# Kernel tuning notes

Measured on AMD Instinct MI355X. Metric: run time of the kernel, lower is better.

## Reference

```python
import jax, jax.numpy as jnp
import numpy as np

EPS = 1e-12

def _sn(w, u):
    # spectral norm, num_svs=1, num_itrs=1, eval mode (power iteration is
    # under no_grad in the original, so sv is a constant w.r.t. autodiff)
    Wm = w.reshape(w.shape[0], -1)          # [out, in*kh*kw]
    v = u @ Wm                               # [1, in*kh*kw]
    v = v / jnp.maximum(jnp.linalg.norm(v), EPS)
    u2 = v @ Wm.T                            # [1, out]
    u2 = u2 / jnp.maximum(jnp.linalg.norm(u2), EPS)
    sv = jnp.squeeze(v @ Wm.T @ u2.T)        # top singular value estimate
    return w / jax.lax.stop_gradient(sv)


def setup_inputs() -> dict:
    key = jax.random.key(0)
    ks = jax.random.split(key, 10)
    B, C, H, W = 32, 512, 64, 64
    Cr = C // 8
    return {
        'x':  jax.random.normal(ks[0], (B, C, H, W), jnp.float32),
        'w1': jax.random.normal(ks[1], (Cr, C, 1, 1), jnp.float32) * 0.05,
        'b1': jax.random.normal(ks[2], (Cr,), jnp.float32) * 0.02,
        'u1': jax.random.normal(ks[3], (1, Cr), jnp.float32),
        'w2': jax.random.normal(ks[4], (C, Cr, 1, 1), jnp.float32) * 0.05,
        'b2': jax.random.normal(ks[5], (C,), jnp.float32) * 0.02,
        'u2': jax.random.normal(ks[6], (1, C), jnp.float32),
        'w3': jax.random.normal(ks[7], (1, 2, 3, 3), jnp.float32) * 0.1,
        'b3': jax.random.normal(ks[8], (1,), jnp.float32) * 0.02,
        'u3': jax.random.normal(ks[9], (1, 1), jnp.float32),
    }


def reference(x, w1, b1, u1, w2, b2, u2, w3, b3, u3):
    # --- channel attention ---
    W1 = _sn(w1, u1).reshape(w1.shape[0], w1.shape[1])   # [Cr, C]
    W2 = _sn(w2, u2).reshape(w2.shape[0], w2.shape[1])   # [C, Cr]
    avg = jnp.mean(x, axis=(2, 3))                        # [B, C]
    mx  = jnp.max(x, axis=(2, 3))                         # [B, C]
    a = jax.nn.relu(avg @ W1.T + b1) @ W2.T + b2          # [B, C]
    m = jax.nn.relu(mx  @ W1.T + b1) @ W2.T + b2          # [B, C]
    s = jax.nn.sigmoid(a + m)
    x = x * s[:, :, None, None]
    # --- spatial attention ---
    ca = jnp.mean(x, axis=1, keepdims=True)               # [B,1,H,W]
    cm = jnp.max(x, axis=1, keepdims=True)                # [B,1,H,W]
    cat = jnp.concatenate([ca, cm], axis=1)               # [B,2,H,W]
    W3 = _sn(w3, u3)
    y = jax.lax.conv_general_dilated(
        cat, W3, window_strides=(1, 1), padding=((1, 1), (1, 1)),
        dimension_numbers=('NCHW', 'OIHW', 'NCHW'))
    y = y + b3.reshape(1, -1, 1, 1)
    return x * jax.nn.sigmoid(y)
```

## Files before the change

### kernel.cpp

```cpp
#include <hip/hip_runtime.h>


#define B_   32
#define C_   512
#define CR_  64
#define HW_  4096
#define WID_ 64
#define EPSF 1e-12f

__device__ __forceinline__ float sigmoidf(float x) {
  return 1.0f / (1.0f + __expf(-x));
}

__global__ __launch_bounds__(256) void pool_kernel(const float* __restrict__ x,
                                                   float* __restrict__ avg,
                                                   float* __restrict__ mx) {
  const int plane = blockIdx.x * 4 + (threadIdx.x >> 6);
  const int lane = threadIdx.x & 63;
  const float4* xp = (const float4*)(x + (size_t)plane * HW_);
  float s = 0.0f, m = -INFINITY;
  #pragma unroll
  for (int q = 0; q < 16; q++) {
    float4 a = xp[q * 64 + lane];
    s += (a.x + a.y) + (a.z + a.w);
    m = fmaxf(m, fmaxf(fmaxf(a.x, a.y), fmaxf(a.z, a.w)));
  }
  #pragma unroll
  for (int o = 32; o > 0; o >>= 1) {
    s += __shfl_down(s, o);
    m = fmaxf(m, __shfl_down(m, o));
  }
  if (lane == 0) {
    avg[plane] = s * (1.0f / HW_);
    mx[plane] = m;
  }
}

__device__ __forceinline__ float block_reduce_sum(float v, float* red) {
  int t = threadIdx.x;
  red[t] = v;
  __syncthreads();
  for (int o = 128; o > 0; o >>= 1) {
    if (t < o) red[t] += red[t + o];
    __syncthreads();
  }
  float r = red[0];
  __syncthreads();
  return r;
}

__global__ __launch_bounds__(256) void mlp_kernel(const float* __restrict__ avg, const float* __restrict__ mx,
                                                  const float* __restrict__ w1, const float* __restrict__ b1,
                                                  const float* __restrict__ u1,
                                                  const float* __restrict__ w2, const float* __restrict__ b2,
                                                  const float* __restrict__ u2,
                                                  float* __restrict__ s) {
  const int b = blockIdx.y;
  const int qtr = blockIdx.x;
  const int t = threadIdx.x;
  __shared__ float v[C_];
  __shared__ float red[256];
  __shared__ float pool2[2][C_];
  __shared__ float hid[2][CR_];

  if (t < CR_) hid[0][t] = u1[t];
  __syncthreads();
  float ax = 0.0f, ay = 0.0f;
  #pragma unroll 8
  for (int i = 0; i < CR_; i++) {
    float ui = hid[0][i];
    float2 wv = *(const float2*)(w1 + (size_t)i * C_ + 2 * t);
    ax += ui * wv.x; ay += ui * wv.y;
  }
  v[2 * t] = ax; v[2 * t + 1] = ay;
  float nv = block_reduce_sum(ax * ax + ay * ay, red);
  float dv = fmaxf(sqrtf(nv), EPSF);
  {
    int i = t >> 2, part = t & 3;
    const float4* wr = (const float4*)(w1 + (size_t)i * C_ + part * 128);
    float acc = 0.0f;
    #pragma unroll 8
    for (int q = 0; q < 32; q++) {
      float4 wv = wr[q];
      int j = part * 128 + 4 * q;
      acc += v[j] * wv.x + v[j + 1] * wv.y + v[j + 2] * wv.z + v[j + 3] * wv.w;
    }
    acc += __shfl_down(acc, 2);
    acc += __shfl_down(acc, 1);
    float q2 = 0.0f;
    if (part == 0) { float a2 = acc / dv; q2 = a2 * a2; }
    nv = block_reduce_sum(q2, red);
  }
  const float inv1 = fmaxf(sqrtf(nv), EPSF) / nv;

  for (int i = t; i < C_; i += 256) pool2[0][i] = u2[i];
  __syncthreads();
  {
    int j = t & 63, ig = t >> 6;
    const float* wp = w2 + (size_t)ig * 128 * CR_ + j;
    float a = 0.0f;
    #pragma unroll 8
    for (int i = 0; i < 128; i++) a += pool2[0][ig * 128 + i] * wp[(size_t)i * CR_];
    red[t] = a;
  }
  __syncthreads();
  if (t < CR_) v[t] = red[t] + red[t + 64] + red[t + 128] + red[t + 192];
  __syncthreads();
  float p = (t < CR_) ? v[t] * v[t] : 0.0f;
  nv = block_reduce_sum(p, red);
  dv = fmaxf(sqrtf(nv), EPSF);
  {
    float q = 0.0f;
    #pragma unroll
    for (int rep = 0; rep < 2; rep++) {
      int i = t + rep * 256;
      const float4* wr = (const float4*)(w2 + (size_t)i * CR_);
      float acc = 0.0f;
      #pragma unroll
      for (int qq = 0; qq < 16; qq++) {
        float4 wv = wr[qq];
        acc += v[4 * qq] * wv.x + v[4 * qq + 1] * wv.y +
               v[4 * qq + 2] * wv.z + v[4 * qq + 3] * wv.w;
      }
      acc /= dv;
      q += acc * acc;
    }
    nv = block_reduce_sum(q, red);
  }
  const float inv2 = fmaxf(sqrtf(nv), EPSF) / nv;

  for (int i = t; i < C_; i += 256) {
    pool2[0][i] = avg[b * C_ + i];
    pool2[1][i] = mx[b * C_ + i];
  }
  __syncthreads();
  if (t < 2 * CR_) {
    int kind = t >> 6;
    int i = t & 63;
    const float4* wr = (const float4*)(w1 + (size_t)i * C_);
    float acc = 0.0f;
    #pragma unroll 8
    for (int qq = 0; qq < C_ / 4; qq++) {
      float4 u = wr[qq];
      acc += pool2[kind][qq * 4 + 0] * u.x + pool2[kind][qq * 4 + 1] * u.y +
             pool2[kind][qq * 4 + 2] * u.z + pool2[kind][qq * 4 + 3] * u.w;
    }
    hid[kind][i] = fmaxf(acc * inv1 + b1[i], 0.0f);
  }
  __syncthreads();
  if (t < 128) {
    int c = qtr * 128 + t;
    const float4* wr = (const float4*)(w2 + (size_t)c * CR_);
    float aa = 0.0f, mm = 0.0f;
    #pragma unroll
    for (int k = 0; k < 16; k++) {
      float4 wv = wr[k];
      aa += hid[0][4 * k] * wv.x + hid[0][4 * k + 1] * wv.y +
            hid[0][4 * k + 2] * wv.z + hid[0][4 * k + 3] * wv.w;
      mm += hid[1][4 * k] * wv.x + hid[1][4 * k + 1] * wv.y +
            hid[1][4 * k + 2] * wv.z + hid[1][4 * k + 3] * wv.w;
    }
    float val = (aa + mm) * inv2 + 2.0f * b2[c];
    s[b * C_ + c] = sigmoidf(val);
  }
}

__global__ __launch_bounds__(256) void scale_pool_kernel(const float* __restrict__ x,
                                                         const float* __restrict__ s,
                                                         float* __restrict__ ca,
                                                         float* __restrict__ cm) {
  const int b = blockIdx.y;
  const int hw0 = blockIdx.x * 128;
  const int t = threadIdx.x;
  const int pxs = t & 31;
  const int cg = t >> 5;
  __shared__ float srow[C_];
  for (int i = t; i < C_; i += 256) srow[i] = s[b * C_ + i];
  __syncthreads();
  const int px = hw0 + pxs * 4;
  const float* xb = x + (size_t)b * C_ * HW_ + px;
  float4 sm = make_float4(0.f, 0.f, 0.f, 0.f);
  float4 mxv = make_float4(-INFINITY, -INFINITY, -INFINITY, -INFINITY);
  const int c0 = cg * 64;
  #pragma unroll 8
  for (int c = c0; c < c0 + 64; c++) {
    float4 u = *(const float4*)(xb + (size_t)c * HW_);
    float sc = srow[c];
    float v0 = u.x * sc, v1 = u.y * sc, v2 = u.z * sc, v3 = u.w * sc;
    sm.x += v0; sm.y += v1; sm.z += v2; sm.w += v3;
    mxv.x = fmaxf(mxv.x, v0); mxv.y = fmaxf(mxv.y, v1);
    mxv.z = fmaxf(mxv.z, v2); mxv.w = fmaxf(mxv.w, v3);
  }
  __shared__ float4 rs[8][32], rm[8][32];
  rs[cg][pxs] = sm; rm[cg][pxs] = mxv;
  __syncthreads();
  if (t < 32) {
    float4 S = rs[0][t], M = rm[0][t];
    #pragma unroll
    for (int g = 1; g < 8; g++) {
      float4 a = rs[g][t], m2 = rm[g][t];
      S.x += a.x; S.y += a.y; S.z += a.z; S.w += a.w;
      M.x = fmaxf(M.x, m2.x); M.y = fmaxf(M.y, m2.y);
      M.z = fmaxf(M.z, m2.z); M.w = fmaxf(M.w, m2.w);
    }
    S.x *= (1.0f / C_); S.y *= (1.0f / C_); S.z *= (1.0f / C_); S.w *= (1.0f / C_);
    *(float4*)(ca + (size_t)b * HW_ + hw0 + t * 4) = S;
    *(float4*)(cm + (size_t)b * HW_ + hw0 + t * 4) = M;
  }
}

__global__ __launch_bounds__(256) void conv_sy_kernel(const float* __restrict__ ca,
                                                      const float* __restrict__ cm,
                                                      const float* __restrict__ w3,
                                                      const float* __restrict__ b3,
                                                      const float* __restrict__ u3,
                                                      float* __restrict__ sy) {
  const int b = blockIdx.y;
  const int hw0 = blockIdx.x * 512;
  const int t = threadIdx.x;
  __shared__ float ssv3;
  if (t == 0) {
    float u3v = u3[0];
    float nvs = 0.0f;
    for (int k = 0; k < 18; k++) { float vv = u3v * w3[k]; nvs += vv * vv; }
    float d = fmaxf(sqrtf(nvs), EPSF);
    float tt = 0.0f;
    for (int k = 0; k < 18; k++) tt += (u3v * w3[k] / d) * w3[k];
    float u2n = tt / fmaxf(fabsf(tt), EPSF);
    ssv3 = tt * u2n;
  }
  __syncthreads();
  const float inv3 = 1.0f / ssv3;
  float wn[18];
  #pragma unroll
  for (int k = 0; k < 18; k++) wn[k] = w3[k] * inv3;
  const float b3f = b3[0];

  #pragma unroll
  for (int e = 0; e < 2; e++) {
    int px = hw0 + t * 2 + e;
    int h = px >> 6, w = px & 63;
    float acc = b3f;
    #pragma unroll
    for (int dh = -1; dh <= 1; dh++) {
      int hh = h + dh;
      if (hh < 0 || hh >= 64) continue;
      #pragma unroll
      for (int dw = -1; dw <= 1; dw++) {
        int ww = w + dw;
        if (ww < 0 || ww >= WID_) continue;
        int n = b * HW_ + hh * WID_ + ww;
        int k = (dh + 1) * 3 + (dw + 1);
        acc += ca[n] * wn[k] + cm[n] * wn[9 + k];
      }
    }
    sy[b * HW_ + px] = sigmoidf(acc);
  }
}

__global__ __launch_bounds__(256) void out_kernel(const float* __restrict__ x,
                                                  const float* __restrict__ s,
                                                  const float* __restrict__ sy,
                                                  float* __restrict__ out) {
  const size_t N4 = (size_t)B_ * C_ * HW_ / 4;
  const size_t stride = (size_t)gridDim.x * blockDim.x;
  for (size_t i = (size_t)blockIdx.x * blockDim.x + threadIdx.x; i < N4; i += stride) {
    size_t base = i * 4;
    int hw = (int)(base & (HW_ - 1));
    int bc = (int)(base >> 12);
    int b  = bc >> 9;
    float sc = s[bc];
    float4 u = ((const float4*)x)[i];
    float4 g = *(const float4*)(sy + (size_t)b * HW_ + hw);
    float4 r;
    r.x = u.x * sc * g.x;
    r.y = u.y * sc * g.y;
    r.z = u.z * sc * g.z;
    r.w = u.w * sc * g.w;
    ((float4*)out)[i] = r;
  }
}

extern "C" void kernel_launch(void* const* d_in, const int* in_sizes, int n_in,
                              void* d_out, int out_size, void* d_ws, size_t ws_size,
                              hipStream_t stream) {
  const float* x  = (const float*)d_in[0];
  const float* w1 = (const float*)d_in[1];
  const float* b1 = (const float*)d_in[2];
  const float* u1 = (const float*)d_in[3];
  const float* w2 = (const float*)d_in[4];
  const float* b2 = (const float*)d_in[5];
  const float* u2 = (const float*)d_in[6];
  const float* w3 = (const float*)d_in[7];
  const float* b3 = (const float*)d_in[8];
  const float* u3 = (const float*)d_in[9];

  float* ws = (float*)d_ws;
  float* avg = ws;
  float* mx  = ws + 16384;
  float* s   = ws + 32768;
  float* ca  = ws + 49152;
  float* cm  = ws + 180224;
  float* sy  = ws + 311296;

  pool_kernel<<<B_ * C_ / 4, 256, 0, stream>>>(x, avg, mx);
  mlp_kernel<<<dim3(4, B_), 256, 0, stream>>>(avg, mx, w1, b1, u1, w2, b2, u2, s);
  scale_pool_kernel<<<dim3(32, B_), 256, 0, stream>>>(x, s, ca, cm);
  conv_sy_kernel<<<dim3(8, B_), 256, 0, stream>>>(ca, cm, w3, b3, u3, sy);
  out_kernel<<<2048, 256, 0, stream>>>(x, s, sy, (float*)d_out);
}
```

Before: 583.7 us.

## Fuse spatial conv with output scaling and parallelize spectral-norm power iterations

Merges the 3x3 spatial conv/sigmoid kernel into the final output kernel, so each block computes its 128-pixel tile of sy in shared memory and then streams x to out with nontemporal vector loads and stores. This removes one launch and the sy round trip through global memory. The MLP kernel also runs the two spectral-norm power iterations concurrently on the two halves of the block, with split reductions that need fewer barriers. The conv work now uses only half the threads per block and repeats the spectral-norm setup in every block.

```diff
diff --git a/kernel.cpp b/kernel.cpp
--- a/kernel.cpp
+++ b/kernel.cpp
@@ -7,6 +7,8 @@
 #define HW_  4096
 #define WID_ 64
 #define EPSF 1e-12f
+
+typedef float f32x4 __attribute__((ext_vector_type(4)));
 
 __device__ __forceinline__ float sigmoidf(float x) {
   return 1.0f / (1.0f + __expf(-x));
@@ -36,19 +38,6 @@
   }
 }
 
-__device__ __forceinline__ float block_reduce_sum(float v, float* red) {
-  int t = threadIdx.x;
-  red[t] = v;
-  __syncthreads();
-  for (int o = 128; o > 0; o >>= 1) {
-    if (t < o) red[t] += red[t + o];
-    __syncthreads();
-  }
-  float r = red[0];
-  __syncthreads();
-  return r;
-}
-
 __global__ __launch_bounds__(256) void mlp_kernel(const float* __restrict__ avg, const float* __restrict__ mx,
                                                   const float* __restrict__ w1, const float* __restrict__ b1,
                                                   const float* __restrict__ u1,
@@ -58,85 +47,104 @@
   const int b = blockIdx.y;
   const int qtr = blockIdx.x;
   const int t = threadIdx.x;
-  __shared__ float v[C_];
+  __shared__ float v1[C_];
+  __shared__ float v2[CR_];
   __shared__ float red[256];
+  __shared__ float part2[128];
+  __shared__ float u1s[CR_];
+  __shared__ float u2s[C_];
   __shared__ float pool2[2][C_];
   __shared__ float hid[2][CR_];
 
-  if (t < CR_) hid[0][t] = u1[t];
-  __syncthreads();
-  float ax = 0.0f, ay = 0.0f;
-  #pragma unroll 8
-  for (int i = 0; i < CR_; i++) {
-    float ui = hid[0][i];
-    float2 wv = *(const float2*)(w1 + (size_t)i * C_ + 2 * t);
-    ax += ui * wv.x; ay += ui * wv.y;
-  }
-  v[2 * t] = ax; v[2 * t + 1] = ay;
-  float nv = block_reduce_sum(ax * ax + ay * ay, red);
-  float dv = fmaxf(sqrtf(nv), EPSF);
-  {
-    int i = t >> 2, part = t & 3;
-    const float4* wr = (const float4*)(w1 + (size_t)i * C_ + part * 128);
+  if (t < CR_) u1s[t] = u1[t];
+  for (int i = t; i < C_; i += 256) {
+    u2s[i] = u2[i];
+    pool2[0][i] = avg[b * C_ + i];
+    pool2[1][i] = mx[b * C_ + i];
+  }
+  __syncthreads();
+
+  float sqp = 0.0f;
+  if (t < 128) {
+    const int j0 = t * 4;
+    float a0 = 0.f, a1 = 0.f, a2 = 0.f, a3 = 0.f;
+    #pragma unroll 8
+    for (int i = 0; i < CR_; i++) {
+      float ui = u1s[i];
+      float4 wv = *(const float4*)(w1 + (size_t)i * C_ + j0);
+      a0 += ui * wv.x; a1 += ui * wv.y; a2 += ui * wv.z; a3 += ui * wv.w;
+    }
+    v1[j0] = a0; v1[j0 + 1] = a1; v1[j0 + 2] = a2; v1[j0 + 3] = a3;
+    sqp = a0 * a0 + a1 * a1 + a2 * a2 + a3 * a3;
+  } else {
+    const int tt = t - 128, j = tt & 63, half = tt >> 6;
+    const float* wp = w2 + (size_t)(half * 256) * CR_ + j;
+    float a = 0.0f;
+    #pragma unroll 8
+    for (int i = 0; i < 256; i++) a += u2s[half * 256 + i] * wp[(size_t)i * CR_];
+    part2[tt] = a;
+  }
+  __syncthreads();
+  if (t >= 128) {
+    const int tt = t - 128;
+    if (tt < CR_) { float vv = part2[tt] + part2[tt + 64]; v2[tt] = vv; sqp = vv * vv; }
+  }
+  red[t] = sqp;
+  __syncthreads();
+  const int rbase = t & 128, ridx = t & 127;
+  #pragma unroll
+  for (int o = 64; o > 0; o >>= 1) {
+    if (ridx < o) red[rbase + ridx] += red[rbase + ridx + o];
+    __syncthreads();
+  }
+  const float dv1 = fmaxf(sqrtf(red[0]), EPSF);
+  const float dv2 = fmaxf(sqrtf(red[128]), EPSF);
+  __syncthreads();
+
+  float sq2 = 0.0f;
+  if (t < 128) {
+    const int i = t >> 1, part = t & 1;
+    const float4* wr = (const float4*)(w1 + (size_t)i * C_ + part * 256);
     float acc = 0.0f;
     #pragma unroll 8
-    for (int q = 0; q < 32; q++) {
+    for (int q = 0; q < 64; q++) {
       float4 wv = wr[q];
-      int j = part * 128 + 4 * q;
-      acc += v[j] * wv.x + v[j + 1] * wv.y + v[j + 2] * wv.z + v[j + 3] * wv.w;
-    }
-    acc += __shfl_down(acc, 2);
+      int j = part * 256 + 4 * q;
+      acc += v1[j] * wv.x + v1[j + 1] * wv.y + v1[j + 2] * wv.z + v1[j + 3] * wv.w;
+    }
     acc += __shfl_down(acc, 1);
-    float q2 = 0.0f;
-    if (part == 0) { float a2 = acc / dv; q2 = a2 * a2; }
-    nv = block_reduce_sum(q2, red);
-  }
-  const float inv1 = fmaxf(sqrtf(nv), EPSF) / nv;
-
-  for (int i = t; i < C_; i += 256) pool2[0][i] = u2[i];
-  __syncthreads();
-  {
-    int j = t & 63, ig = t >> 6;
-    const float* wp = w2 + (size_t)ig * 128 * CR_ + j;
-    float a = 0.0f;
-    #pragma unroll 8
-    for (int i = 0; i < 128; i++) a += pool2[0][ig * 128 + i] * wp[(size_t)i * CR_];
-    red[t] = a;
-  }
-  __syncthreads();
-  if (t < CR_) v[t] = red[t] + red[t + 64] + red[t + 128] + red[t + 192];
-  __syncthreads();
-  float p = (t < CR_) ? v[t] * v[t] : 0.0f;
-  nv = block_reduce_sum(p, red);
-  dv = fmaxf(sqrtf(nv), EPSF);
-  {
-    float q = 0.0f;
+    if (part == 0) { float a2 = acc / dv1; sq2 = a2 * a2; }
+  } else {
+    const int tt = t - 128;
     #pragma unroll
-    for (int rep = 0; rep < 2; rep++) {
-      int i = t + rep * 256;
+    for (int r = 0; r < 4; r++) {
+      const int i = tt * 4 + r;
       const float4* wr = (const float4*)(w2 + (size_t)i * CR_);
       float acc = 0.0f;
       #pragma unroll
-      for (int qq = 0; qq < 16; qq++) {
-        float4 wv = wr[qq];
-        acc += v[4 * qq] * wv.x + v[4 * qq + 1] * wv.y +
-               v[4 * qq + 2] * wv.z + v[4 * qq + 3] * wv.w;
+      for (int q = 0; q < 16; q++) {
+        float4 wv = wr[q];
+        acc += v2[4 * q] * wv.x + v2[4 * q + 1] * wv.y +
+               v2[4 * q + 2] * wv.z + v2[4 * q + 3] * wv.w;
       }
-      acc /= dv;
-      q += acc * acc;
-    }
-    nv = block_reduce_sum(q, red);
-  }
-  const float inv2 = fmaxf(sqrtf(nv), EPSF) / nv;
-
-  for (int i = t; i < C_; i += 256) {
-    pool2[0][i] = avg[b * C_ + i];
-    pool2[1][i] = mx[b * C_ + i];
-  }
-  __syncthreads();
+      acc /= dv2;
+      sq2 += acc * acc;
+    }
+  }
+  red[t] = sq2;
+  __syncthreads();
+  #pragma unroll
+  for (int o = 64; o > 0; o >>= 1) {
+    if (ridx < o) red[rbase + ridx] += red[rbase + ridx + o];
+    __syncthreads();
+  }
+  const float nt1 = red[0], nt2 = red[128];
+  const float inv1 = fmaxf(sqrtf(nt1), EPSF) / nt1;
+  const float inv2 = fmaxf(sqrtf(nt2), EPSF) / nt2;
+  __syncthreads();
+
   if (t < 2 * CR_) {
-    int kind = t >> 6;
-    int i = t & 63;
+    const int kind = t >> 6, i = t & 63;
     const float4* wr = (const float4*)(w1 + (size_t)i * C_);
     float acc = 0.0f;
     #pragma unroll 8
@@ -149,7 +157,7 @@
   }
   __syncthreads();
   if (t < 128) {
-    int c = qtr * 128 + t;
+    const int c = qtr * 128 + t;
     const float4* wr = (const float4*)(w2 + (size_t)c * CR_);
     float aa = 0.0f, mm = 0.0f;
     #pragma unroll
@@ -209,16 +217,21 @@
   }
 }
 
-__global__ __launch_bounds__(256) void conv_sy_kernel(const float* __restrict__ ca,
-                                                      const float* __restrict__ cm,
-                                                      const float* __restrict__ w3,
-                                                      const float* __restrict__ b3,
-                                                      const float* __restrict__ u3,
-                                                      float* __restrict__ sy) {
+__global__ __launch_bounds__(256) void conv_out_kernel(const float* __restrict__ x,
+                                                       const float* __restrict__ s,
+                                                       const float* __restrict__ ca,
+                                                       const float* __restrict__ cm,
+                                                       const float* __restrict__ w3,
+                                                       const float* __restrict__ b3,
+                                                       const float* __restrict__ u3,
+                                                       float* __restrict__ out) {
   const int b = blockIdx.y;
-  const int hw0 = blockIdx.x * 512;
+  const int hw0 = blockIdx.x * 128;
   const int t = threadIdx.x;
-  __shared__ float ssv3;
+  __shared__ float srow[C_];
+  __shared__ __align__(16) float syt[128];
+  __shared__ float wns[18];
+  __shared__ float b3s;
   if (t == 0) {
     float u3v = u3[0];
     float nvs = 0.0f;
@@ -227,20 +240,16 @@
     float tt = 0.0f;
     for (int k = 0; k < 18; k++) tt += (u3v * w3[k] / d) * w3[k];
     float u2n = tt / fmaxf(fabsf(tt), EPSF);
-    ssv3 = tt * u2n;
-  }
-  __syncthreads();
-  const float inv3 = 1.0f / ssv3;
-  float wn[18];
-  #pragma unroll
-  for (int k = 0; k < 18; k++) wn[k] = w3[k] * inv3;
-  const float b3f = b3[0];
-
-  #pragma unroll
-  for (int e = 0; e < 2; e++) {
-    int px = hw0 + t * 2 + e;
-    int h = px >> 6, w = px & 63;
-    float acc = b3f;
+    float inv3 = 1.0f / (tt * u2n);
+    for (int k = 0; k < 18; k++) wns[k] = w3[k] * inv3;
+    b3s = b3[0];
+  }
+  for (int i = t; i < C_; i += 256) srow[i] = s[b * C_ + i];
+  __syncthreads();
+  if (t < 128) {
+    const int px = hw0 + t;
+    const int h = px >> 6, w = px & 63;
+    float acc = b3s;
     #pragma unroll
     for (int dh = -1; dh <= 1; dh++) {
       int hh = h + dh;
@@ -251,33 +260,22 @@
         if (ww < 0 || ww >= WID_) continue;
         int n = b * HW_ + hh * WID_ + ww;
         int k = (dh + 1) * 3 + (dw + 1);
-        acc += ca[n] * wn[k] + cm[n] * wn[9 + k];
+        acc += ca[n] * wns[k] + cm[n] * wns[9 + k];
       }
     }
-    sy[b * HW_ + px] = sigmoidf(acc);
-  }
-}
-
-__global__ __launch_bounds__(256) void out_kernel(const float* __restrict__ x,
-                                                  const float* __restrict__ s,
-                                                  const float* __restrict__ sy,
-                                                  float* __restrict__ out) {
-  const size_t N4 = (size_t)B_ * C_ * HW_ / 4;
-  const size_t stride = (size_t)gridDim.x * blockDim.x;
-  for (size_t i = (size_t)blockIdx.x * blockDim.x + threadIdx.x; i < N4; i += stride) {
-    size_t base = i * 4;
-    int hw = (int)(base & (HW_ - 1));
-    int bc = (int)(base >> 12);
-    int b  = bc >> 9;
-    float sc = s[bc];
-    float4 u = ((const float4*)x)[i];
-    float4 g = *(const float4*)(sy + (size_t)b * HW_ + hw);
-    float4 r;
-    r.x = u.x * sc * g.x;
-    r.y = u.y * sc * g.y;
-    r.z = u.z * sc * g.z;
-    r.w = u.w * sc * g.w;
-    ((float4*)out)[i] = r;
+    syt[t] = sigmoidf(acc);
+  }
+  __syncthreads();
+  const int pxs = t & 31;
+  const int cg = t >> 5;
+  const f32x4 sy4 = *(const f32x4*)(&syt[pxs * 4]);
+  const size_t base = (size_t)b * C_ * HW_ + hw0 + pxs * 4;
+  const int c0 = cg * 64;
+  #pragma unroll 8
+  for (int c = c0; c < c0 + 64; c++) {
+    const f32x4 u = __builtin_nontemporal_load((const f32x4*)(x + base + (size_t)c * HW_));
+    const f32x4 r = u * (srow[c] * sy4);
+    __builtin_nontemporal_store(r, (f32x4*)(out + base + (size_t)c * HW_));
   }
 }
 
@@ -301,11 +299,9 @@
   float* s   = ws + 32768;
   float* ca  = ws + 49152;
   float* cm  = ws + 180224;
-  float* sy  = ws + 311296;
 
   pool_kernel<<<B_ * C_ / 4, 256, 0, stream>>>(x, avg, mx);
   mlp_kernel<<<dim3(4, B_), 256, 0, stream>>>(avg, mx, w1, b1, u1, w2, b2, u2, s);
   scale_pool_kernel<<<dim3(32, B_), 256, 0, stream>>>(x, s, ca, cm);
-  conv_sy_kernel<<<dim3(8, B_), 256, 0, stream>>>(ca, cm, w3, b3, u3, sy);
-  out_kernel<<<2048, 256, 0, stream>>>(x, s, sy, (float*)d_out);
-}
+  conv_out_kernel<<<dim3(32, B_), 256, 0, stream>>>(x, s, ca, cm, w3, b3, u3, (float*)d_out);
+}
```

Result: faster. 562.5 us (-3.6%).
